# Kernel tuning notes

Measured on AMD Instinct MI355X. Metric: run time of the kernel, lower is better.

## Reference

```python
import jax, jax.numpy as jnp
import numpy as np

N = 50000
E = 250000
NUM_ETYPES = 4
H = 2  # num_heads
EPS = 1e-12


def _gat_conv(x, W, al, ar, b, src, dst):
    # x: (N, in_dim); W: (in_dim, H*D); al/ar/b: (H, D); src/dst: (E,)
    D = al.shape[-1]
    feat = (x @ W).reshape(-1, H, D)            # (N, H, D)
    el = jnp.sum(feat * al, axis=-1)            # (N, H)
    er = jnp.sum(feat * ar, axis=-1)            # (N, H)
    e = jax.nn.leaky_relu(el[src] + er[dst], 0.2)   # (E, H)
    emax = jax.ops.segment_max(e, dst, num_segments=N)
    ex = jnp.exp(e - emax[dst])
    denom = jax.ops.segment_sum(ex, dst, num_segments=N)
    alpha = ex / denom[dst]                     # (E, H) segment softmax over in-edges
    msg = feat[src] * alpha[:, :, None]         # (E, H, D)
    out = jax.ops.segment_sum(msg, dst, num_segments=N)  # (N, H, D)
    return out + b


def _hetero_layer(x, W, al, ar, b, edges):
    # vmap GATConv over the edge-type axis, then HeteroGraphConv aggregate='mean'
    outs = jax.vmap(lambda w, a, r, bb, e: _gat_conv(x, w, a, r, bb, e[0], e[1]))(
        W, al, ar, b, edges)                    # (T, N, H, D)
    return jnp.mean(outs, axis=0)               # (N, H, D)


def _post(v):
    # relu -> F.normalize(dim=1, i.e. across heads) -> dropout(eval: identity) -> mean over heads
    v = jax.nn.relu(v)
    norm = jnp.sqrt(jnp.sum(v * v, axis=1, keepdims=True))
    v = v / jnp.maximum(norm, EPS)
    return jnp.mean(v, axis=1)                  # (N, D)


def setup_inputs() -> dict:
    key = jax.random.key(0)
    ks = jax.random.split(key, 16)
    s = 0.05
    inp = {
        'x': jax.random.normal(ks[0], (N, 23), jnp.float32),
        'edges': jax.random.randint(ks[1], (NUM_ETYPES, 2, E), 0, N, jnp.int32),
        'W0': jax.random.normal(ks[2], (NUM_ETYPES, 23, H * 64), jnp.float32) * s,
        'al0': jax.random.normal(ks[3], (NUM_ETYPES, H, 64), jnp.float32) * s,
        'ar0': jax.random.normal(ks[4], (NUM_ETYPES, H, 64), jnp.float32) * s,
        'b0': jnp.zeros((NUM_ETYPES, H, 64), jnp.float32),
        'W1': jax.random.normal(ks[5], (NUM_ETYPES, 64, H * 64), jnp.float32) * s,
        'al1': jax.random.normal(ks[6], (NUM_ETYPES, H, 64), jnp.float32) * s,
        'ar1': jax.random.normal(ks[7], (NUM_ETYPES, H, 64), jnp.float32) * s,
        'b1': jnp.zeros((NUM_ETYPES, H, 64), jnp.float32),
        'W2': jax.random.normal(ks[8], (NUM_ETYPES, 64, H * 64), jnp.float32) * s,
        'al2': jax.random.normal(ks[9], (NUM_ETYPES, H, 64), jnp.float32) * s,
        'ar2': jax.random.normal(ks[10], (NUM_ETYPES, H, 64), jnp.float32) * s,
        'b2': jnp.zeros((NUM_ETYPES, H, 64), jnp.float32),
    }
    return inp


def reference(x, edges, W0, al0, ar0, b0, W1, al1, ar1, b1, W2, al2, ar2, b2):
    h = x  # feature_by_level, feat_level=0
    h = _post(_hetero_layer(h, W0, al0, ar0, b0, edges))
    h = _post(_hetero_layer(h, W1, al1, ar1, b1, edges))
    h = jnp.mean(_hetero_layer(h, W2, al2, ar2, b2, edges), axis=1)  # (N, out_dim)
    out = jnp.mean(h, axis=0, keepdims=True)    # dgl.mean_nodes, single graph -> (1, out_dim)
    return out
```

## Files before the change

kernel.cpp:

```cpp
#include <hip/hip_runtime.h>

#define NN 50000
#define NE 250000
#define NSCAN_BLKS ((NN + 255)/256)
#define EDGE_BLKS ((4*NE + 255)/256)

typedef __attribute__((ext_vector_type(8))) short bf16x8;
typedef __attribute__((ext_vector_type(4))) float f32x4;

__device__ inline ushort f2bf(float f) {
  uint u = __float_as_uint(f);
  return (ushort)((u + 0x7fffu + ((u >> 16) & 1u)) >> 16);
}
__device__ inline float bf2f(ushort b) { return __uint_as_float(((uint)b) << 16); }

__global__ __launch_bounds__(256) void zero_ints(int* __restrict__ p, int n) {
  int i = blockIdx.x*256 + threadIdx.x;
  if (i < n) p[i] = 0;
}
__global__ __launch_bounds__(256) void zero_floats(float* __restrict__ p, int n) {
  int i = blockIdx.x*256 + threadIdx.x;
  if (i < n) p[i] = 0.f;
}

__global__ __launch_bounds__(256) void count_kernel(const int* __restrict__ edges, int* __restrict__ counts) {
  int idx = blockIdx.x*256 + threadIdx.x;
  if (idx >= 4*NE) return;
  int t = idx / NE, e = idx - t*NE;
  int dst = edges[(size_t)t*2*NE + NE + e];
  atomicAdd(&counts[t*NN + dst], 1);
}

__global__ __launch_bounds__(256) void sumdeg_kernel(const int* __restrict__ counts, int* __restrict__ totdeg) {
  int v = blockIdx.x*256 + threadIdx.x;
  if (v < NN) totdeg[v] = counts[v] + counts[NN+v] + counts[2*NN+v] + counts[3*NN+v];
}

__global__ __launch_bounds__(256) void scan1_kernel(const int* __restrict__ in, int* __restrict__ out, int* __restrict__ bsum, int n) {
  __shared__ int sd[256];
  int i = blockIdx.x*256 + threadIdx.x;
  int v = (i < n) ? in[i] : 0;
  sd[threadIdx.x] = v;
  __syncthreads();
  for (int off = 1; off < 256; off <<= 1) {
    int add = (threadIdx.x >= off) ? sd[threadIdx.x - off] : 0;
    __syncthreads();
    sd[threadIdx.x] += add;
    __syncthreads();
  }
  if (i < n) out[i] = sd[threadIdx.x] - v;
  if (threadIdx.x == 255) bsum[blockIdx.x] = sd[255];
}

__global__ __launch_bounds__(1024) void scan2_kernel(int* __restrict__ bsum, int nb) {
  __shared__ int sd[1024];
  int i = threadIdx.x;
  int v = (i < nb) ? bsum[i] : 0;
  sd[i] = v;
  __syncthreads();
  for (int off = 1; off < 1024; off <<= 1) {
    int add = (i >= off) ? sd[i - off] : 0;
    __syncthreads();
    sd[i] += add;
    __syncthreads();
  }
  if (i < nb) bsum[i] = sd[i] - v;
}

__global__ __launch_bounds__(256) void scan3b_kernel(int* __restrict__ rp, const int* __restrict__ bsum, int n, int total) {
  int i = blockIdx.x*256 + threadIdx.x;
  if (i < n) rp[i] += bsum[blockIdx.x];
  if (i == 0) rp[n] = total;
}

__global__ __launch_bounds__(256) void make_cursor_kernel(const int* __restrict__ rp2, const int* __restrict__ counts,
                                                          int* __restrict__ cursor, int* __restrict__ sub_ptr) {
  int v = blockIdx.x*256 + threadIdx.x;
  if (v >= NN) return;
  int b = rp2[v];
  int s1 = b  + counts[v];
  int s2 = s1 + counts[NN+v];
  int s3 = s2 + counts[2*NN+v];
  cursor[v] = b; cursor[NN+v] = s1; cursor[2*NN+v] = s2; cursor[3*NN+v] = s3;
  sub_ptr[NN+v] = s1; sub_ptr[2*NN+v] = s2; sub_ptr[3*NN+v] = s3;
}

__global__ __launch_bounds__(256) void scatter2_kernel(const int* __restrict__ edges, int* __restrict__ cursor,
                                                       int* __restrict__ col2, int* __restrict__ posmap) {
  int idx = blockIdx.x*256 + threadIdx.x;
  if (idx >= 4*NE) return;
  int t = idx / NE, e = idx - t*NE;
  int src = edges[(size_t)t*2*NE + e];
  int dst = edges[(size_t)t*2*NE + NE + e];
  int pos = atomicAdd(&cursor[t*NN + dst], 1);
  col2[pos] = t*NN + src;
  posmap[idx] = pos;
}

__global__ __launch_bounds__(256) void convert_x_kernel(const float* __restrict__ x, ushort* __restrict__ xpad) {
  int i = blockIdx.x*256 + threadIdx.x;
  if (i >= NN*64) return;
  int k = i & 63, n = i >> 6;
  xpad[i] = (k < 23) ? f2bf(x[n*23 + k]) : (ushort)0;
}

__global__ __launch_bounds__(256) void convert_wt2_kernel(const float* __restrict__ W, const float* __restrict__ al,
                                                          const float* __restrict__ ar, ushort* __restrict__ WTg2, int Kin) {
  int i = blockIdx.x*256 + threadIdx.x;
  if (i >= 4*144*64) return;
  int k = i & 63; int c = (i >> 6) % 144; int t = i / (144*64);
  float val = 0.f;
  if (c < 128) {
    val = (k < Kin) ? W[((size_t)t*Kin + k)*128 + c] : 0.f;
  } else if (c < 132 && k < Kin) {
    int m = c - 128, h = m & 1;
    const float* A = ((m < 2) ? al : ar) + t*128 + h*64;
    const float* wrow = W + ((size_t)t*Kin + k)*128 + h*64;
    float s = 0.f;
    for (int c2 = 0; c2 < 64; ++c2) s += wrow[c2]*A[c2];
    val = s;
  }
  WTg2[((size_t)t*144 + c)*64 + k] = f2bf(val);
}

__global__ __launch_bounds__(256)
void gemm_mfma_kernel(const ushort* __restrict__ hbf,
                      const ushort* __restrict__ WTg2,
                      uint* __restrict__ featu,
                      float* __restrict__ elr)
{
  __shared__ ushort WT[144*64];
  const int t = blockIdx.y;
  const int tid = threadIdx.x;
  const int wv = tid >> 6, lane = tid & 63;
  const int node0 = blockIdx.x*64;

  {
    const ushort* src = WTg2 + (size_t)t*144*64;
    for (int i = tid; i < 1152; i += 256) {
      int c = i >> 3, jj = i & 7;
      bf16x8 val = *(const bf16x8*)(src + (size_t)c*64 + jj*8);
      *(bf16x8*)((char*)WT + c*128 + ((jj ^ (c & 7))*16)) = val;
    }
  }
  __syncthreads();

  const int mrow = lane & 15;
  const int kq = lane >> 4;
  const int anode = node0 + wv*16 + mrow;

  const bf16x8 a0 = *(const bf16x8*)(hbf + (size_t)anode*64 + kq*8);
  const bf16x8 a1 = *(const bf16x8*)(hbf + (size_t)anode*64 + 32 + kq*8);

  f32x4 acc[9];
  #pragma unroll
  for (int nb = 0; nb < 9; ++nb) acc[nb] = (f32x4){0.f,0.f,0.f,0.f};

  #pragma unroll
  for (int nb = 0; nb < 9; ++nb) {
    const int c = nb*16 + mrow;
    const bf16x8 b0 = *(const bf16x8*)((const char*)WT + c*128 + ((kq       ^ (c&7))*16));
    const bf16x8 b1 = *(const bf16x8*)((const char*)WT + c*128 + (((4 + kq) ^ (c&7))*16));
    acc[nb] = __builtin_amdgcn_mfma_f32_16x16x32_bf16(a0, b0, acc[nb], 0, 0, 0);
    acc[nb] = __builtin_amdgcn_mfma_f32_16x16x32_bf16(a1, b1, acc[nb], 0, 0, 0);
  }

  const int noder = node0 + wv*16 + kq*4;
  #pragma unroll
  for (int nb = 0; nb < 4; ++nb) {
    const int d = nb*16 + mrow;
    #pragma unroll
    for (int r = 0; r < 4; ++r) {
      if (noder + r < NN) {
        const uint pk = (uint)f2bf(acc[nb][r]) | ((uint)f2bf(acc[nb+4][r]) << 16);
        featu[((size_t)t*NN + noder + r)*64 + d] = pk;
      }
    }
  }
  if (mrow < 4) {
    #pragma unroll
    for (int r = 0; r < 4; ++r) {
      if (noder + r < NN)
        elr[(size_t)(mrow*4 + t)*NN + noder + r] = acc[8][r];
    }
  }
}

__global__ __launch_bounds__(256)
void phaseA_kernel(const int* __restrict__ edges, const float* __restrict__ elr,
                   const int* __restrict__ posmap, float* __restrict__ pexp)
{
  int idx = blockIdx.x*256 + threadIdx.x;
  if (idx >= 4*NE) return;
  int t = idx / NE, e = idx - t*NE;
  int src = edges[(size_t)t*2*NE + e];
  int dst = edges[(size_t)t*2*NE + NE + e];
  float u0 = elr[(size_t)(0*4+t)*NN + src] + elr[(size_t)(2*4+t)*NN + dst];
  float u1 = elr[(size_t)(1*4+t)*NN + src] + elr[(size_t)(3*4+t)*NN + dst];
  u0 = (u0 > 0.f) ? u0 : 0.2f*u0;
  u1 = (u1 > 0.f) ? u1 : 0.2f*u1;
  float p0 = __expf(fminf(fmaxf(u0, -60.f), 60.f));
  float p1 = __expf(fminf(fmaxf(u1, -60.f), 60.f));
  int pos = posmap[idx];
  ((float2*)pexp)[pos] = make_float2(p0, p1);
}

__global__ __launch_bounds__(256)
void gather_kernel(const uint* __restrict__ featu, const float* __restrict__ pexp,
                   const int* __restrict__ col2, const int* __restrict__ row_ptr2,
                   const int* __restrict__ sub_ptr, const float* __restrict__ ball,
                   ushort* __restrict__ hout, int post)
{
  const int v = __builtin_amdgcn_readfirstlane(blockIdx.x*4 + (threadIdx.x >> 6));
  const int lane = threadIdx.x & 63;

  const int b0 = row_ptr2[v];
  const int b4 = row_ptr2[v+1];
  const int s1 = sub_ptr[NN+v], s2 = sub_ptr[2*NN+v], s3 = sub_ptr[3*NN+v];
  const int bounds[5] = {b0, s1, s2, s3, b4};

  float ax = 0.f, ay = 0.f;

  #pragma unroll
  for (int t = 0; t < 4; ++t) {
    const int lo = bounds[t], hi = bounds[t+1];
    if (lo >= hi) continue;
    float sum0 = 0.f, sum1 = 0.f, tx = 0.f, ty = 0.f;
    #pragma unroll 4
    for (int q = lo; q < hi; ++q) {
      const int c = col2[q];
      const float2 p = ((const float2*)pexp)[q];
      sum0 += p.x; sum1 += p.y;
      const uint w = featu[(uint)c*64u + (uint)lane];
      tx += p.x * __uint_as_float(w << 16);
      ty += p.y * __uint_as_float(w & 0xffff0000u);
    }
    ax += tx * __builtin_amdgcn_rcpf(sum0);
    ay += ty * __builtin_amdgcn_rcpf(sum1);
  }

  float bx = 0.f, by = 0.f;
  #pragma unroll
  for (int t = 0; t < 4; ++t) { bx += ball[t*128 + lane]; by += ball[t*128 + 64 + lane]; }
  ax = 0.25f*(ax + bx); ay = 0.25f*(ay + by);

  float o;
  if (post) {
    ax = fmaxf(ax, 0.f); ay = fmaxf(ay, 0.f);
    o = 0.5f*(ax + ay) / fmaxf(sqrtf(ax*ax + ay*ay), 1e-12f);
  } else {
    o = 0.5f*(ax + ay);
  }
  hout[(size_t)v*64 + lane] = f2bf(o);
}

__global__ __launch_bounds__(256) void reduce_nodes(const ushort* __restrict__ hn, float* __restrict__ accum) {
  __shared__ float sd[256];
  int d = threadIdx.x & 63, rg = threadIdx.x >> 6;
  float s = 0.f;
  for (int r = blockIdx.x*4 + rg; r < NN; r += gridDim.x*4) s += bf2f(hn[(size_t)r*64 + d]);
  sd[threadIdx.x] = s;
  __syncthreads();
  if (threadIdx.x < 64) {
    s = sd[threadIdx.x] + sd[threadIdx.x+64] + sd[threadIdx.x+128] + sd[threadIdx.x+192];
    atomicAdd(&accum[threadIdx.x], s);
  }
}
__global__ __launch_bounds__(64) void final_out_kernel(const float* __restrict__ accum, float* __restrict__ out) {
  int d = threadIdx.x;
  if (d < 64) out[d] = accum[d] * (1.0f/NN);
}

extern "C" void kernel_launch(void* const* d_in, const int* in_sizes, int n_in,
                              void* d_out, int out_size, void* d_ws, size_t ws_size,
                              hipStream_t stream) {
  const float* x     = (const float*)d_in[0];
  const int*   edges = (const int*)d_in[1];
  const float* W[3]  = {(const float*)d_in[2], (const float*)d_in[6], (const float*)d_in[10]};
  const float* al[3] = {(const float*)d_in[3], (const float*)d_in[7], (const float*)d_in[11]};
  const float* ar[3] = {(const float*)d_in[4], (const float*)d_in[8], (const float*)d_in[12]};
  const float* b[3]  = {(const float*)d_in[5], (const float*)d_in[9], (const float*)d_in[13]};

  char* ws = (char*)d_ws;
  auto up = [](size_t x_) { return (x_ + 255) & ~(size_t)255; };

  const size_t szFeat = (size_t)4*NN*64*sizeof(uint);
  const size_t szElr  = (size_t)16*NN*sizeof(float);
  const size_t szPex  = (size_t)4*NE*2*sizeof(float);
  const size_t szPM   = (size_t)4*NE*sizeof(int);
  const size_t szHB   = (size_t)(NN+64)*64*sizeof(ushort);
  const size_t szWT   = (size_t)4*144*64*sizeof(ushort);
  const size_t szI4   = (size_t)4*NN*sizeof(int);
  const size_t szI1   = (size_t)(NN+1)*sizeof(int);

  size_t o = 0;
  uint*   featu  = (uint*)(ws + o);   o += up(szFeat);
  float*  elr    = (float*)(ws + o);  o += up(szElr);
  float*  pexp   = (float*)(ws + o);  o += up(szPex);
  int*    posmap = (int*)(ws + o);    o += up(szPM);
  int*    col2   = (int*)(ws + o);    o += up(szPM);
  ushort* xpad   = (ushort*)(ws + o); o += up(szHB);
  ushort* hbuf   = (ushort*)(ws + o); o += up(szHB);
  ushort* WTg2   = (ushort*)(ws + o); o += up(szWT);
  float*  accum  = (float*)(ws + o);  o += up(256);
  int* row_ptr2  = (int*)(ws + o);    o += up(szI1);
  int* totdeg    = (int*)(ws + o);    o += up(szI1);
  int* cursor    = (int*)(ws + o);    o += up(szI4);
  int* counts    = (int*)(ws + o);    o += up(szI4);
  int* sub_ptr   = (int*)(ws + o);    o += up(szI4);
  int* bsum      = (int*)(ws + o);    o += up(4096);

  zero_ints<<<(4*NN + 255)/256, 256, 0, stream>>>(counts, 4*NN);
  count_kernel<<<EDGE_BLKS, 256, 0, stream>>>(edges, counts);
  sumdeg_kernel<<<NSCAN_BLKS, 256, 0, stream>>>(counts, totdeg);
  scan1_kernel<<<NSCAN_BLKS, 256, 0, stream>>>(totdeg, row_ptr2, bsum, NN);
  scan2_kernel<<<1, 1024, 0, stream>>>(bsum, NSCAN_BLKS);
  scan3b_kernel<<<NSCAN_BLKS, 256, 0, stream>>>(row_ptr2, bsum, NN, 4*NE);
  make_cursor_kernel<<<NSCAN_BLKS, 256, 0, stream>>>(row_ptr2, counts, cursor, sub_ptr);
  scatter2_kernel<<<EDGE_BLKS, 256, 0, stream>>>(edges, cursor, col2, posmap);

  convert_x_kernel<<<(NN*64 + 255)/256, 256, 0, stream>>>(x, xpad);

  const int gemmGX = (NN + 63)/64;

  for (int l = 0; l < 3; ++l) {
    const ushort* hin = (l == 0) ? xpad : hbuf;
    convert_wt2_kernel<<<(4*144*64 + 255)/256, 256, 0, stream>>>(W[l], al[l], ar[l], WTg2, (l == 0) ? 23 : 64);
    gemm_mfma_kernel<<<dim3(gemmGX, 4), 256, 0, stream>>>(hin, WTg2, featu, elr);
    phaseA_kernel<<<EDGE_BLKS, 256, 0, stream>>>(edges, elr, posmap, pexp);
    gather_kernel<<<NN/4, 256, 0, stream>>>(featu, pexp, col2, row_ptr2, sub_ptr, b[l], hbuf, (l < 2) ? 1 : 0);
  }

  zero_floats<<<1, 64, 0, stream>>>(accum, 64);
  reduce_nodes<<<256, 256, 0, stream>>>(hbuf, accum);
  final_out_kernel<<<1, 64, 0, stream>>>(accum, (float*)d_out);
}
```

Before: 428.4 us.

## Fuse edge attention scores into gather kernel, drop posmap and pexp buffers

```diff
diff --git a/kernel.cpp b/kernel.cpp
--- a/kernel.cpp
+++ b/kernel.cpp
@@ -86,7 +86,7 @@
 }
 
 __global__ __launch_bounds__(256) void scatter2_kernel(const int* __restrict__ edges, int* __restrict__ cursor,
-                                                       int* __restrict__ col2, int* __restrict__ posmap) {
+                                                       int* __restrict__ col2) {
   int idx = blockIdx.x*256 + threadIdx.x;
   if (idx >= 4*NE) return;
   int t = idx / NE, e = idx - t*NE;
@@ -94,7 +94,6 @@
   int dst = edges[(size_t)t*2*NE + NE + e];
   int pos = atomicAdd(&cursor[t*NN + dst], 1);
   col2[pos] = t*NN + src;
-  posmap[idx] = pos;
 }
 
 __global__ __launch_bounds__(256) void convert_x_kernel(const float* __restrict__ x, ushort* __restrict__ xpad) {
@@ -127,7 +126,7 @@
 void gemm_mfma_kernel(const ushort* __restrict__ hbf,
                       const ushort* __restrict__ WTg2,
                       uint* __restrict__ featu,
-                      float* __restrict__ elr)
+                      float* __restrict__ elp, float* __restrict__ erp)
 {
   __shared__ ushort WT[144*64];
   const int t = blockIdx.y;
@@ -178,38 +177,21 @@
     }
   }
   if (mrow < 4) {
+    const int h = mrow & 1;
+    float* dstp = (mrow < 2) ? elp : erp;
     #pragma unroll
     for (int r = 0; r < 4; ++r) {
       if (noder + r < NN)
-        elr[(size_t)(mrow*4 + t)*NN + noder + r] = acc[8][r];
+        dstp[((size_t)t*NN + noder + r)*2 + h] = acc[8][r];
     }
   }
 }
 
 __global__ __launch_bounds__(256)
-void phaseA_kernel(const int* __restrict__ edges, const float* __restrict__ elr,
-                   const int* __restrict__ posmap, float* __restrict__ pexp)
-{
-  int idx = blockIdx.x*256 + threadIdx.x;
-  if (idx >= 4*NE) return;
-  int t = idx / NE, e = idx - t*NE;
-  int src = edges[(size_t)t*2*NE + e];
-  int dst = edges[(size_t)t*2*NE + NE + e];
-  float u0 = elr[(size_t)(0*4+t)*NN + src] + elr[(size_t)(2*4+t)*NN + dst];
-  float u1 = elr[(size_t)(1*4+t)*NN + src] + elr[(size_t)(3*4+t)*NN + dst];
-  u0 = (u0 > 0.f) ? u0 : 0.2f*u0;
-  u1 = (u1 > 0.f) ? u1 : 0.2f*u1;
-  float p0 = __expf(fminf(fmaxf(u0, -60.f), 60.f));
-  float p1 = __expf(fminf(fmaxf(u1, -60.f), 60.f));
-  int pos = posmap[idx];
-  ((float2*)pexp)[pos] = make_float2(p0, p1);
-}
-
-__global__ __launch_bounds__(256)
-void gather_kernel(const uint* __restrict__ featu, const float* __restrict__ pexp,
-                   const int* __restrict__ col2, const int* __restrict__ row_ptr2,
-                   const int* __restrict__ sub_ptr, const float* __restrict__ ball,
-                   ushort* __restrict__ hout, int post)
+void gather_kernel(const uint* __restrict__ featu, const float* __restrict__ elp,
+                   const float* __restrict__ erp, const int* __restrict__ col2,
+                   const int* __restrict__ row_ptr2, const int* __restrict__ sub_ptr,
+                   const float* __restrict__ ball, ushort* __restrict__ hout, int post)
 {
   const int v = __builtin_amdgcn_readfirstlane(blockIdx.x*4 + (threadIdx.x >> 6));
   const int lane = threadIdx.x & 63;
@@ -225,15 +207,21 @@
   for (int t = 0; t < 4; ++t) {
     const int lo = bounds[t], hi = bounds[t+1];
     if (lo >= hi) continue;
+    const float2 er2 = ((const float2*)erp)[(size_t)t*NN + v];
     float sum0 = 0.f, sum1 = 0.f, tx = 0.f, ty = 0.f;
     #pragma unroll 4
     for (int q = lo; q < hi; ++q) {
       const int c = col2[q];
-      const float2 p = ((const float2*)pexp)[q];
-      sum0 += p.x; sum1 += p.y;
+      const float2 e2 = ((const float2*)elp)[c];
+      float u0 = e2.x + er2.x, u1 = e2.y + er2.y;
+      u0 = (u0 > 0.f) ? u0 : 0.2f*u0;
+      u1 = (u1 > 0.f) ? u1 : 0.2f*u1;
+      const float p0 = __expf(fminf(fmaxf(u0, -60.f), 60.f));
+      const float p1 = __expf(fminf(fmaxf(u1, -60.f), 60.f));
+      sum0 += p0; sum1 += p1;
       const uint w = featu[(uint)c*64u + (uint)lane];
-      tx += p.x * __uint_as_float(w << 16);
-      ty += p.y * __uint_as_float(w & 0xffff0000u);
+      tx += p0 * __uint_as_float(w << 16);
+      ty += p1 * __uint_as_float(w & 0xffff0000u);
     }
     ax += tx * __builtin_amdgcn_rcpf(sum0);
     ay += ty * __builtin_amdgcn_rcpf(sum1);
@@ -285,9 +273,8 @@
   auto up = [](size_t x_) { return (x_ + 255) & ~(size_t)255; };
 
   const size_t szFeat = (size_t)4*NN*64*sizeof(uint);
-  const size_t szElr  = (size_t)16*NN*sizeof(float);
-  const size_t szPex  = (size_t)4*NE*2*sizeof(float);
-  const size_t szPM   = (size_t)4*NE*sizeof(int);
+  const size_t szElp  = (size_t)4*NN*2*sizeof(float);
+  const size_t szCol  = (size_t)4*NE*sizeof(int);
   const size_t szHB   = (size_t)(NN+64)*64*sizeof(ushort);
   const size_t szWT   = (size_t)4*144*64*sizeof(ushort);
   const size_t szI4   = (size_t)4*NN*sizeof(int);
@@ -295,10 +282,9 @@
 
   size_t o = 0;
   uint*   featu  = (uint*)(ws + o);   o += up(szFeat);
-  float*  elr    = (float*)(ws + o);  o += up(szElr);
-  float*  pexp   = (float*)(ws + o);  o += up(szPex);
-  int*    posmap = (int*)(ws + o);    o += up(szPM);
-  int*    col2   = (int*)(ws + o);    o += up(szPM);
+  float*  elp    = (float*)(ws + o);  o += up(szElp);
+  float*  erp    = (float*)(ws + o);  o += up(szElp);
+  int*    col2   = (int*)(ws + o);    o += up(szCol);
   ushort* xpad   = (ushort*)(ws + o); o += up(szHB);
   ushort* hbuf   = (ushort*)(ws + o); o += up(szHB);
   ushort* WTg2   = (ushort*)(ws + o); o += up(szWT);
@@ -317,7 +303,7 @@
   scan2_kernel<<<1, 1024, 0, stream>>>(bsum, NSCAN_BLKS);
   scan3b_kernel<<<NSCAN_BLKS, 256, 0, stream>>>(row_ptr2, bsum, NN, 4*NE);
   make_cursor_kernel<<<NSCAN_BLKS, 256, 0, stream>>>(row_ptr2, counts, cursor, sub_ptr);
-  scatter2_kernel<<<EDGE_BLKS, 256, 0, stream>>>(edges, cursor, col2, posmap);
+  scatter2_kernel<<<EDGE_BLKS, 256, 0, stream>>>(edges, cursor, col2);
 
   convert_x_kernel<<<(NN*64 + 255)/256, 256, 0, stream>>>(x, xpad);
 
@@ -326,9 +312,8 @@
   for (int l = 0; l < 3; ++l) {
     const ushort* hin = (l == 0) ? xpad : hbuf;
     convert_wt2_kernel<<<(4*144*64 + 255)/256, 256, 0, stream>>>(W[l], al[l], ar[l], WTg2, (l == 0) ? 23 : 64);
-    gemm_mfma_kernel<<<dim3(gemmGX, 4), 256, 0, stream>>>(hin, WTg2, featu, elr);
-    phaseA_kernel<<<EDGE_BLKS, 256, 0, stream>>>(edges, elr, posmap, pexp);
-    gather_kernel<<<NN/4, 256, 0, stream>>>(featu, pexp, col2, row_ptr2, sub_ptr, b[l], hbuf, (l < 2) ? 1 : 0);
+    gemm_mfma_kernel<<<dim3(gemmGX, 4), 256, 0, stream>>>(hin, WTg2, featu, elp, erp);
+    gather_kernel<<<NN/4, 256, 0, stream>>>(featu, elp, erp, col2, row_ptr2, sub_ptr, b[l], hbuf, (l < 2) ? 1 : 0);
   }
 
   zero_floats<<<1, 64, 0, stream>>>(accum, 64);
```

Measured after the change: 409.5 us. 4.4% less time.
